# Kernel tuning notes

Measured on AMD Instinct MI355X. Metric: run time of the kernel, lower is better.

Reference implementation:

```python
import jax, jax.numpy as jnp
import numpy as np

B, C, H, W = 8, 3, 1080, 1920
K = 256        # number of CRF sample points
NB = 25        # number of PCA basis curves (EMoR-style)


def setup_inputs() -> dict:
    key = jax.random.key(0)
    k1, k2, k3, k4 = jax.random.split(key, 4)
    hdr_image = jax.random.uniform(k1, (B, C, H, W), dtype=jnp.float32)
    weights_w = jax.random.normal(k2, (B, NB), dtype=jnp.float32) * 0.1
    # np.interp requires strictly increasing sample points
    E_samples = jnp.sort(jax.random.uniform(k3, (K,), dtype=jnp.float32))
    # monotone base camera-response curve + small random basis
    f0_mean = jnp.linspace(0.0, 1.0, K, dtype=jnp.float32)
    H_basis = jax.random.normal(k4, (K, NB), dtype=jnp.float32) * 0.05
    return {"hdr_image": hdr_image, "weights_w": weights_w,
            "E_samples": E_samples, "f0_mean": f0_mean, "H_basis": H_basis}


def reference(hdr_image, weights_w, E_samples, f0_mean, H_basis):
    # curve_delta = (H_basis @ weights_w.T).T -> [B, K]
    CRF_curve = f0_mean + jnp.einsum('kn,bn->bk', H_basis, weights_w)
    # per-batch piecewise-linear LUT lookup over all C*H*W pixels at once
    # (jnp.interp matches np.interp: clamps below E_samples[0] / above E_samples[-1])
    def interp_one(img_chw, curve_k):
        return jnp.interp(img_chw, E_samples, curve_k)
    sdr = jax.vmap(interp_one)(hdr_image, CRF_curve)  # [B, C, H, W]
    return jnp.clip(sdr, 0.0, 1.0)
```

## Files before the change

kernel.cpp:

```cpp
#include <hip/hip_runtime.h>


#define KS 256
#define NB 25
#define M_BINS 4096
#define BINS_PER_THR (M_BINS / 256)
#define NPIX_PER_B 6220800
#define NP4 (NPIX_PER_B / 4)

__device__ __forceinline__ float interp_one(float x,
                                            const float* __restrict__ sE,
                                            const float4* __restrict__ sT,
                                            const unsigned short* __restrict__ sBkt)
{
    int m = (int)(x * 4096.0f);
    m = (m > M_BINS - 1) ? (M_BINS - 1) : m;
    int j = sBkt[m];
    while (j < KS && sE[j] <= x) ++j;
    float4 t = sT[j];
    float y = fmaf(t.z, x - t.x, t.y);
    return fminf(fmaxf(y, 0.0f), 1.0f);
}

__global__ __launch_bounds__(256, 8)
void tmo_lut_kernel(const float* __restrict__ hdr,
                    const float* __restrict__ w,
                    const float* __restrict__ E,
                    const float* __restrict__ f0,
                    const float* __restrict__ Hb,
                    float* __restrict__ out)
{
    __shared__ float sE[KS];
    __shared__ float sC[KS];
    __shared__ float4 sT[KS + 1];
    __shared__ unsigned short sBkt[M_BINS];

    const int tid = threadIdx.x;
    const int b   = blockIdx.y;

    sE[tid] = E[tid];
    {
        float acc = f0[tid];
        const float* wb = w + b * NB;
        const float* hb = Hb + tid * NB;
        #pragma unroll
        for (int n = 0; n < NB; ++n) acc = fmaf(hb[n], wb[n], acc);
        sC[tid] = acc;
    }
    __syncthreads();

    if (tid == 0) {
        sT[0]  = make_float4(sE[0],      sC[0],      0.0f, 0.0f);
        sT[KS] = make_float4(sE[KS - 1], sC[KS - 1], 0.0f, 0.0f);
    } else {
        float e0 = sE[tid - 1], e1 = sE[tid];
        float c0 = sC[tid - 1], c1 = sC[tid];
        float sl = (c1 - c0) / (e1 - e0);
        sT[tid] = make_float4(e0, c0, sl, 0.0f);
    }

    {
        const float invM = 1.0f / (float)M_BINS;
        int m0 = tid * BINS_PER_THR;
        float v0 = (float)m0 * invM;
        int lo = 0, hi = KS;
        while (lo < hi) {
            int mid = (lo + hi) >> 1;
            if (sE[mid] <= v0) lo = mid + 1; else hi = mid;
        }
        int j = lo;
        for (int m = m0; m < m0 + BINS_PER_THR; ++m) {
            float mv = (float)m * invM;
            while (j < KS && sE[j] <= mv) ++j;
            sBkt[m] = (unsigned short)j;
        }
    }
    __syncthreads();

    const float4* in4  = (const float4*)(hdr + (size_t)b * NPIX_PER_B);
    float4*       out4 = (float4*)(out + (size_t)b * NPIX_PER_B);

    const int stride = gridDim.x * blockDim.x;
    for (int i = blockIdx.x * blockDim.x + tid; i < NP4; i += stride) {
        float4 p = in4[i];
        float4 r;
        r.x = interp_one(p.x, sE, sT, sBkt);
        r.y = interp_one(p.y, sE, sT, sBkt);
        r.z = interp_one(p.z, sE, sT, sBkt);
        r.w = interp_one(p.w, sE, sT, sBkt);
        out4[i] = r;
    }
}

extern "C" void kernel_launch(void* const* d_in, const int* in_sizes, int n_in,
                              void* d_out, int out_size, void* d_ws, size_t ws_size,
                              hipStream_t stream)
{
    const float* hdr = (const float*)d_in[0];
    const float* w   = (const float*)d_in[1];
    const float* E   = (const float*)d_in[2];
    const float* f0  = (const float*)d_in[3];
    const float* Hb  = (const float*)d_in[4];
    float* out = (float*)d_out;

    dim3 grid(256, 8, 1);
    dim3 block(256, 1, 1);
    tmo_lut_kernel<<<grid, block, 0, stream>>>(hdr, w, E, f0, Hb, out);
}
```

Before: 344.1 us.

## Pack bucket bounds, use slope-intercept segments, unroll loads and nontemporal stores

Each bucket entry now packs the start index together with a bounded count of breakpoints inside the bucket, so the per-pixel linear search stops early without checking the array end. Segments are stored as float2 slope/intercept pairs instead of float4 records, which halves LDS reads per lookup and drops a subtraction. The main loop is unrolled 4x to issue four global loads before computing, and outputs use nontemporal stores to avoid polluting cache. The intercept form may differ slightly in rounding from the original x-e0 formulation, and the count saturates at 127.

```diff
diff --git a/kernel.cpp b/kernel.cpp
--- a/kernel.cpp
+++ b/kernel.cpp
@@ -8,17 +8,29 @@
 #define NPIX_PER_B 6220800
 #define NP4 (NPIX_PER_B / 4)
 
+typedef float nvec4 __attribute__((ext_vector_type(4)));
+
+__device__ __forceinline__ void nt_store4(float4* dst, float4 v)
+{
+    __builtin_nontemporal_store(*(const nvec4*)&v, (nvec4*)dst);
+}
+
 __device__ __forceinline__ float interp_one(float x,
                                             const float* __restrict__ sE,
-                                            const float4* __restrict__ sT,
+                                            const float2* __restrict__ sSeg,
                                             const unsigned short* __restrict__ sBkt)
 {
-    int m = (int)(x * 4096.0f);
+    int m = (int)(x * (float)M_BINS);
     m = (m > M_BINS - 1) ? (M_BINS - 1) : m;
-    int j = sBkt[m];
-    while (j < KS && sE[j] <= x) ++j;
-    float4 t = sT[j];
-    float y = fmaf(t.z, x - t.x, t.y);
+    unsigned int pk = sBkt[m];
+    unsigned int j  = pk & 0x1FFu;
+    unsigned int c  = pk >> 9;
+    while (c) {
+        if (sE[j] > x) break;
+        ++j; --c;
+    }
+    float2 sg = sSeg[j];
+    float y = fmaf(sg.x, x, sg.y);
     return fminf(fmaxf(y, 0.0f), 1.0f);
 }
 
@@ -30,9 +42,9 @@
                     const float* __restrict__ Hb,
                     float* __restrict__ out)
 {
-    __shared__ float sE[KS];
-    __shared__ float sC[KS];
-    __shared__ float4 sT[KS + 1];
+    __shared__ float  sE[KS];
+    __shared__ float  sC[KS];
+    __shared__ float2 sSeg[KS + 1];
     __shared__ unsigned short sBkt[M_BINS];
 
     const int tid = threadIdx.x;
@@ -50,45 +62,80 @@
     __syncthreads();
 
     if (tid == 0) {
-        sT[0]  = make_float4(sE[0],      sC[0],      0.0f, 0.0f);
-        sT[KS] = make_float4(sE[KS - 1], sC[KS - 1], 0.0f, 0.0f);
+        sSeg[0]  = make_float2(0.0f, sC[0]);
+        sSeg[KS] = make_float2(0.0f, sC[KS - 1]);
     } else {
         float e0 = sE[tid - 1], e1 = sE[tid];
         float c0 = sC[tid - 1], c1 = sC[tid];
         float sl = (c1 - c0) / (e1 - e0);
-        sT[tid] = make_float4(e0, c0, sl, 0.0f);
+        float bi = fmaf(-sl, e0, c0);
+        sSeg[tid] = make_float2(sl, bi);
     }
 
     {
-        const float invM = 1.0f / (float)M_BINS;
+        const float h = 1.0f / (float)M_BINS;
         int m0 = tid * BINS_PER_THR;
-        float v0 = (float)m0 * invM;
+        float v0 = (float)m0 * h;
         int lo = 0, hi = KS;
         while (lo < hi) {
             int mid = (lo + hi) >> 1;
             if (sE[mid] <= v0) lo = mid + 1; else hi = mid;
         }
         int j = lo;
-        for (int m = m0; m < m0 + BINS_PER_THR; ++m) {
-            float mv = (float)m * invM;
-            while (j < KS && sE[j] <= mv) ++j;
-            sBkt[m] = (unsigned short)j;
+        for (int t = 0; t < BINS_PER_THR; ++t) {
+            int m = m0 + t;
+            float vn = (float)(m + 1) * h;
+            int jn = j;
+            while (jn < KS && sE[jn] <= vn) ++jn;
+            int c = jn - j;
+            c = (c > 127) ? 127 : c;
+            sBkt[m] = (unsigned short)(j | (c << 9));
+            j = jn;
         }
     }
     __syncthreads();
 
-    const float4* in4  = (const float4*)(hdr + (size_t)b * NPIX_PER_B);
-    float4*       out4 = (float4*)(out + (size_t)b * NPIX_PER_B);
+    const float4* __restrict__ in4 = (const float4*)(hdr + (size_t)b * NPIX_PER_B);
+    float4*                   out4 = (float4*)(out + (size_t)b * NPIX_PER_B);
 
     const int stride = gridDim.x * blockDim.x;
-    for (int i = blockIdx.x * blockDim.x + tid; i < NP4; i += stride) {
+    int i = blockIdx.x * blockDim.x + tid;
+
+    for (; i + 3 * stride < NP4; i += 4 * stride) {
+        float4 p0 = in4[i];
+        float4 p1 = in4[i +     stride];
+        float4 p2 = in4[i + 2 * stride];
+        float4 p3 = in4[i + 3 * stride];
+        float4 r;
+        r.x = interp_one(p0.x, sE, sSeg, sBkt);
+        r.y = interp_one(p0.y, sE, sSeg, sBkt);
+        r.z = interp_one(p0.z, sE, sSeg, sBkt);
+        r.w = interp_one(p0.w, sE, sSeg, sBkt);
+        nt_store4(&out4[i], r);
+        r.x = interp_one(p1.x, sE, sSeg, sBkt);
+        r.y = interp_one(p1.y, sE, sSeg, sBkt);
+        r.z = interp_one(p1.z, sE, sSeg, sBkt);
+        r.w = interp_one(p1.w, sE, sSeg, sBkt);
+        nt_store4(&out4[i + stride], r);
+        r.x = interp_one(p2.x, sE, sSeg, sBkt);
+        r.y = interp_one(p2.y, sE, sSeg, sBkt);
+        r.z = interp_one(p2.z, sE, sSeg, sBkt);
+        r.w = interp_one(p2.w, sE, sSeg, sBkt);
+        nt_store4(&out4[i + 2 * stride], r);
+        r.x = interp_one(p3.x, sE, sSeg, sBkt);
+        r.y = interp_one(p3.y, sE, sSeg, sBkt);
+        r.z = interp_one(p3.z, sE, sSeg, sBkt);
+        r.w = interp_one(p3.w, sE, sSeg, sBkt);
+        nt_store4(&out4[i + 3 * stride], r);
+    }
+    for (; i < NP4; i += stride) {
         float4 p = in4[i];
         float4 r;
-        r.x = interp_one(p.x, sE, sT, sBkt);
-        r.y = interp_one(p.y, sE, sT, sBkt);
-        r.z = interp_one(p.z, sE, sT, sBkt);
-        r.w = interp_one(p.w, sE, sT, sBkt);
-        out4[i] = r;
+        r.x = interp_one(p.x, sE, sSeg, sBkt);
+        r.y = interp_one(p.y, sE, sSeg, sBkt);
+        r.z = interp_one(p.z, sE, sSeg, sBkt);
+        r.w = interp_one(p.w, sE, sSeg, sBkt);
+        nt_store4(&out4[i], r);
     }
 }
 
```

Result: no change. 337.4 us (-1.9%).
